# Optimization experiments

Hardware: AMD Instinct MI355X
Metric: run time of the kernel (lower is better)

The kernel has to match this reference:

```python
import jax, jax.numpy as jnp
import numpy as np

NUM_HEADS = 16
ROPE_BASE = 10000.0


def rotate_half(x):
    d = x.shape[-1] // 2
    return jnp.concatenate([-x[..., d:], x[..., :d]], axis=-1)


def setup_inputs() -> dict:
    key = jax.random.key(0)
    ks = jax.random.split(key, 6)
    B, S, H = 2, 2048, 1024
    scale = 1.0 / np.sqrt(H)  # ~xavier for square matrices
    x = jax.random.normal(ks[0], (B, S, H), dtype=jnp.float32)
    Wq = jax.random.normal(ks[1], (H, H), dtype=jnp.float32) * scale
    Wk = jax.random.normal(ks[2], (H, H), dtype=jnp.float32) * scale
    Wv = jax.random.normal(ks[3], (H, H), dtype=jnp.float32) * scale
    Wo = jax.random.normal(ks[4], (H, H), dtype=jnp.float32) * scale
    # learnable bias, tril-initialized as in the torch module
    bias = jnp.tril(jax.random.normal(ks[5], (S, S), dtype=jnp.float32) * 0.02)
    return {"x": x, "Wq": Wq, "Wk": Wk, "Wv": Wv, "Wo": Wo, "bias": bias}


def reference(x, Wq, Wk, Wv, Wo, bias):
    B, S, H = x.shape
    nh = NUM_HEADS
    hd = H // nh

    # projections (torch Linear: y = x @ W.T), split heads -> [B, nh, S, hd]
    q = (x @ Wq.T).reshape(B, S, nh, hd).transpose(0, 2, 1, 3)
    k = (x @ Wk.T).reshape(B, S, nh, hd).transpose(0, 2, 1, 3)
    v = (x @ Wv.T).reshape(B, S, nh, hd).transpose(0, 2, 1, 3)

    # rotary embeddings, position_ids = arange(S)
    inv_freq = 1.0 / (ROPE_BASE ** (jnp.arange(0, hd, 2, dtype=jnp.float32) / hd))
    t = jnp.arange(S, dtype=jnp.float32)
    freqs = t[:, None] * inv_freq[None, :]          # [S, hd/2]
    emb = jnp.concatenate([freqs, freqs], axis=-1)  # [S, hd]
    cos = jnp.cos(emb).astype(x.dtype)
    sin = jnp.sin(emb).astype(x.dtype)
    q = q * cos + rotate_half(q) * sin
    k = k * cos + rotate_half(k) * sin

    # scores + learnable bias + causal mask
    scores = jnp.einsum('bhqd,bhkd->bhqk', q, k) / np.float32(np.sqrt(hd))
    scores = scores + bias[:S, :S][None, None, :, :]
    causal = jnp.tril(jnp.ones((S, S), dtype=bool))
    scores = jnp.where(causal, scores, -jnp.inf)

    attn = jax.nn.softmax(scores, axis=-1)
    out = jnp.einsum('bhqk,bhkd->bhqd', attn, v)
    out = out.transpose(0, 2, 1, 3).reshape(B, S, H)
    return out @ Wo.T, attn
```

## Files before the change

### kernel.cpp

```cpp
#include <hip/hip_runtime.h>
#include <hip/hip_bf16.h>
#include <math.h>


typedef __attribute__((ext_vector_type(8))) short bx8;
typedef __attribute__((ext_vector_type(4))) short sx4;
typedef __attribute__((ext_vector_type(4))) float fx4;
typedef __attribute__((ext_vector_type(4))) float f4v;

#define MFMA_BF16(a, b, c) __builtin_amdgcn_mfma_f32_16x16x32_bf16(a, b, c, 0, 0, 0)
#define LOG2E 1.44269504088896340736f

__device__ __forceinline__ short f2bf(float f) {
    union { float f; unsigned u; } v; v.f = f;
    unsigned u = v.u;
    u += 0x7fffu + ((u >> 16) & 1u);
    return (short)(u >> 16);
}

__device__ __forceinline__ bx8 pack8(f4v a, f4v b) {
    bx8 r;
    r[0] = f2bf(a[0]); r[1] = f2bf(a[1]); r[2] = f2bf(a[2]); r[3] = f2bf(a[3]);
    r[4] = f2bf(b[0]); r[5] = f2bf(b[1]); r[6] = f2bf(b[2]); r[7] = f2bf(b[3]);
    return r;
}

__device__ __forceinline__ void gload_lds16(const short* g, short* l) {
    __builtin_amdgcn_global_load_lds(
        (const __attribute__((address_space(1))) void*)g,
        (__attribute__((address_space(3))) void*)l, 16, 0, 0);
}

__global__ __launch_bounds__(256) void cast_kernel(
        const float* __restrict__ x, const float* __restrict__ Wq,
        const float* __restrict__ Wk, const float* __restrict__ Wv,
        const float* __restrict__ Wo, const float* __restrict__ bias,
        short* __restrict__ dst, float* __restrict__ biasF)
{
    const size_t M1 = 1u << 20;
    if (blockIdx.x < 4096) {
        const size_t e0 = ((size_t)blockIdx.x * 256 + threadIdx.x) * 8;
        const float* src; size_t off;
        if (e0 < 4 * M1) { src = x; off = e0; }
        else {
            const int j = (int)((e0 - 4 * M1) >> 20);
            src = (j == 0) ? Wq : (j == 1) ? Wk : (j == 2) ? Wv : Wo;
            off = (e0 - 4 * M1) & (M1 - 1);
        }
        f4v a = *(const f4v*)(src + off);
        f4v b = *(const f4v*)(src + off + 4);
        *(bx8*)(dst + e0) = pack8(a, b);
    } else {
        const size_t e0 = ((size_t)(blockIdx.x - 4096) * 256 + threadIdx.x) * 8;
        f4v a = *(const f4v*)(bias + e0);
        f4v b = *(const f4v*)(bias + e0 + 4);
        #pragma unroll
        for (int i = 0; i < 4; ++i) { a[i] *= LOG2E; b[i] *= LOG2E; }
        *(f4v*)(biasF + e0) = a;
        *(f4v*)(biasF + e0 + 4) = b;
    }
}

__global__ void rope_table_kernel(float* __restrict__ cosT, float* __restrict__ sinT) {
    int i = blockIdx.x * 256 + threadIdx.x;
    if (i >= 2048 * 64) return;
    int s = i >> 6, d = i & 63;
    int fi = d & 31;
    float inv_freq = powf(10000.0f, -(float)fi / 32.0f);
    float ang = (float)s * inv_freq;
    cosT[i] = cosf(ang);
    sinT[i] = sinf(ang);
}

template<int OUTPROJ>
__global__ __launch_bounds__(256) void gemm128(
        const short* __restrict__ A, const short* __restrict__ W0,
        const short* __restrict__ W1, const short* __restrict__ W2,
        const float* __restrict__ cosT, const float* __restrict__ sinT,
        void* __restrict__ Out)
{
    __shared__ short As[128][64];
    __shared__ short Bs[128][64];
    const int bm = blockIdx.x, bn = blockIdx.y, z = blockIdx.z;
    const short* W = OUTPROJ ? W0 : (z == 0 ? W0 : (z == 1 ? W1 : W2));
    const int tid = threadIdx.x, w = tid >> 6, lane = tid & 63;
    const int cl = lane & 15, lg = lane >> 4;
    const int srow = lane >> 3;
    const int schunk = (lane & 7) ^ srow;

    fx4 acc[4][4];
    #pragma unroll
    for (int mi = 0; mi < 4; ++mi)
        #pragma unroll
        for (int ni = 0; ni < 4; ++ni) acc[mi][ni] = (fx4){0.f, 0.f, 0.f, 0.f};

    const int wr = (w >> 1) * 64, wc = (w & 1) * 64;

    for (int k0 = 0; k0 < 1024; k0 += 64) {
        __syncthreads();
        #pragma unroll
        for (int i = 0; i < 4; ++i) {
            const int rbase = w * 32 + i * 8;
            gload_lds16(A + (size_t)(bm * 128 + rbase + srow) * 1024 + k0 + schunk * 8,
                        &As[rbase][0]);
            gload_lds16(W + (size_t)(bn * 128 + rbase + srow) * 1024 + k0 + schunk * 8,
                        &Bs[rbase][0]);
        }
        __syncthreads();
        #pragma unroll
        for (int kk = 0; kk < 2; ++kk) {
            bx8 af[4], bf[4];
            #pragma unroll
            for (int i = 0; i < 4; ++i) {
                const int ra = wr + i * 16 + cl;
                af[i] = *(const bx8*)&As[ra][((kk * 4 + lg) ^ (ra & 7)) * 8];
                const int rb = wc + i * 16 + cl;
                bf[i] = *(const bx8*)&Bs[rb][((kk * 4 + lg) ^ (rb & 7)) * 8];
            }
            #pragma unroll
            for (int mi = 0; mi < 4; ++mi)
                #pragma unroll
                for (int ni = 0; ni < 4; ++ni)
                    acc[mi][ni] = MFMA_BF16(af[mi], bf[ni], acc[mi][ni]);
        }
    }

    #pragma unroll
    for (int mi = 0; mi < 4; ++mi) {
        #pragma unroll
        for (int reg = 0; reg < 4; ++reg) {
            const int r = bm * 128 + wr + mi * 16 + (lg << 2) + reg;
            if constexpr (OUTPROJ) {
                #pragma unroll
                for (int ni = 0; ni < 4; ++ni) {
                    const int col = bn * 128 + wc + ni * 16 + cl;
                    ((float*)Out)[(size_t)r * 1024 + col] = acc[mi][ni][reg];
                }
            } else {
                const int b = r >> 11, s = r & 2047;
                const int h = bn * 2 + (wc >> 6);
                short* dst = (short*)Out + (size_t)z * 32 * 2048 * 64
                           + (size_t)((b * 16 + h) * 2048 + s) * 64;
                #pragma unroll
                for (int ni = 0; ni < 4; ++ni) {
                    const int d = ni * 16 + cl;
                    float v = acc[mi][ni][reg];
                    if (z <= 1) {
                        const float cs = cosT[s * 64 + d], sn = sinT[s * 64 + d];
                        const float partner = acc[mi][ni ^ 2][reg];
                        const float rot = (d < 32) ? -partner : partner;
                        v = v * cs + rot * sn;
                        if (z == 0) v *= 0.125f * LOG2E;
                    }
                    dst[d] = f2bf(v);
                }
            }
        }
    }
}

__global__ __launch_bounds__(256, 3) void attn_kernel(
        const short* __restrict__ Q, const short* __restrict__ K,
        const short* __restrict__ V, const float* __restrict__ biasF,
        float* __restrict__ attn_out, short* __restrict__ o_buf)
{
    const int S = 2048;
    const int bid = blockIdx.x;
    const int xcd = bid & 7, rr_ = bid >> 3;
    const int bh = xcd * 4 + (rr_ & 3);
    const int qt = 31 - (rr_ >> 2);
    const int h = bh & 15, b = bh >> 4;
    const int tid = threadIdx.x, w = tid >> 6, lane = tid & 63;
    const int cl = lane & 15, lg = lane >> 4;
    const size_t base = (size_t)bh * S * 64;
    const int NT = qt + 1;

    __shared__ short Ks[2][64][64];
    __shared__ short Vt[2][64][72];
    __shared__ short P[4][16][72];

    const int krow8 = lane >> 3, kchk = (lane & 7) ^ krow8;
    const int vrow = tid >> 2, vd0 = (tid & 3) * 16;

    const short* qp = Q + base + (size_t)(qt * 64 + w * 16 + cl) * 64 + lg * 8;
    const bx8 qf0 = *(const bx8*)qp;
    const bx8 qf1 = *(const bx8*)(qp + 32);
    const int qr  = qt * 64 + w * 16 + cl;
    const int sq0 = qt * 64 + w * 16 + (lg << 2);
    const float* brow = biasF + (size_t)qr * 2048;
    const size_t arow_base = ((size_t)bh * S + qr) * S;

#define STAGEK(BUF, t)                                                            \
    { gload_lds16(K + base + (size_t)((t) * 64 + w * 16 + krow8) * 64 + kchk * 8, \
                  &Ks[BUF][w * 16][0]);                                           \
      gload_lds16(K + base + (size_t)((t) * 64 + w * 16 + 8 + krow8) * 64 + kchk * 8, \
                  &Ks[BUF][w * 16 + 8][0]); }

#define LOADB(BR, t)                                                              \
    { _Pragma("unroll") for (int n = 0; n < 4; ++n)                               \
        BR[n] = *(const f4v*)(brow + (t) * 64 + n * 16 + (lg << 2)); }

#define QKT(BUF, BR, SACC)                                                        \
    { const int cs_ = cl & 7;                                                     \
      _Pragma("unroll") for (int n = 0; n < 4; ++n) {                             \
        bx8 a0 = *(const bx8*)&Ks[BUF][n * 16 + cl][(lg ^ cs_) * 8];              \
        bx8 a1 = *(const bx8*)&Ks[BUF][n * 16 + cl][((4 + lg) ^ cs_) * 8];        \
        SACC[n] = MFMA_BF16(a0, qf0, BR[n]);                                      \
        SACC[n] = MFMA_BF16(a1, qf1, SACC[n]); } }

#define COMP_A(BUF, BR, t)                                                        \
    { fx4 sacc[4]; QKT(BUF, BR, sacc);                                            \
      _Pragma("unroll") for (int n = 0; n < 4; ++n)                               \
        _Pragma("unroll") for (int e = 0; e < 4; ++e) {                           \
          const int kc = (t) * 64 + n * 16 + (lg << 2) + e;                       \
          lsum[n] += (kc <= qr) ? exp2f(sacc[n][e]) : 0.f; } }

#define LOADVr(V0, V1, t)                                                         \
    { const short* vp = V + base + (size_t)((t) * 64 + vrow) * 64 + vd0;          \
      V0 = *(const bx8*)vp; V1 = *(const bx8*)(vp + 8); }

#define VSTORE(V0, V1, BUF)                                                       \
    { _Pragma("unroll") for (int j = 0; j < 8; ++j) Vt[BUF][vd0 + j][vrow] = V0[j]; \
      _Pragma("unroll") for (int j = 0; j < 8; ++j) Vt[BUF][vd0 + 8 + j][vrow] = V1[j]; }

#define COMP_B(KBUF, BR, VBUF, t)                                                 \
    { fx4 sacc[4]; QKT(KBUF, BR, sacc);                                           \
      float p[4][4];                                                              \
      _Pragma("unroll") for (int n = 0; n < 4; ++n)                               \
        _Pragma("unroll") for (int e = 0; e < 4; ++e) {                           \
          const int kc = (t) * 64 + n * 16 + (lg << 2) + e;                       \
          p[n][e] = (kc <= qr) ? exp2f(sacc[n][e] - L2) : 0.f; }                  \
      _Pragma("unroll") for (int n = 0; n < 4; ++n) {                             \
        f4v st = (f4v){p[n][0], p[n][1], p[n][2], p[n][3]};                       \
        *(f4v*)(attn_out + arow_base + (t) * 64 + n * 16 + (lg << 2)) = st;       \
        sx4 pb;                                                                   \
        pb[0] = f2bf(p[n][0]); pb[1] = f2bf(p[n][1]);                             \
        pb[2] = f2bf(p[n][2]); pb[3] = f2bf(p[n][3]);                             \
        *(sx4*)&P[w][cl][n * 16 + (lg << 2)] = pb; }                              \
      _Pragma("unroll") for (int kk = 0; kk < 2; ++kk) {                          \
        bx8 pa = *(const bx8*)&P[w][cl][kk * 32 + lg * 8];                        \
        _Pragma("unroll") for (int n = 0; n < 4; ++n) {                           \
          bx8 vb = *(const bx8*)&Vt[VBUF][n * 16 + cl][kk * 32 + lg * 8];         \
          oacc[n] = MFMA_BF16(pa, vb, oacc[n]); } } }

    float lsum[4] = {0.f, 0.f, 0.f, 0.f};
    f4v bA[4], bB[4];

    STAGEK(0, 0); LOADB(bA, 0);
    __syncthreads();
    int t = 0;
    for (; t + 1 < NT; t += 2) {
        STAGEK(1, t + 1); LOADB(bB, t + 1);
        COMP_A(0, bA, t);
        __syncthreads();
        if (t + 2 < NT) { STAGEK(0, t + 2); LOADB(bA, t + 2); }
        COMP_A(1, bB, t + 1);
        __syncthreads();
    }
    if (t < NT) COMP_A(0, bA, t);

    float l = (lsum[0] + lsum[1]) + (lsum[2] + lsum[3]);
    l += __shfl_xor(l, 16);
    l += __shfl_xor(l, 32);
    const float L2 = __log2f(l);

    fx4 oacc[4];
    #pragma unroll
    for (int n = 0; n < 4; n++) oacc[n] = (fx4){0.f, 0.f, 0.f, 0.f};

    bx8 vA0, vA1, vB0, vB1;
    __syncthreads();
    STAGEK(0, 0); LOADB(bA, 0); LOADVr(vA0, vA1, 0);
    __syncthreads();
    VSTORE(vA0, vA1, 0);
    __syncthreads();
    t = 0;
    for (; t + 1 < NT; t += 2) {
        STAGEK(1, t + 1); LOADB(bB, t + 1); LOADVr(vB0, vB1, t + 1);
        COMP_B(0, bA, 0, t);
        VSTORE(vB0, vB1, 1);
        __syncthreads();
        if (t + 2 < NT) { STAGEK(0, t + 2); LOADB(bA, t + 2); LOADVr(vA0, vA1, t + 2); }
        COMP_B(1, bB, 1, t + 1);
        if (t + 2 < NT) VSTORE(vA0, vA1, 0);
        __syncthreads();
    }
    if (t < NT) COMP_B(0, bA, 0, t);

    #pragma unroll
    for (int reg = 0; reg < 4; reg++) {
        const int sq = sq0 + reg;
        #pragma unroll
        for (int n = 0; n < 4; n++) {
            const int d = n * 16 + cl;
            o_buf[(size_t)(b * 2048 + sq) * 1024 + h * 64 + d] = f2bf(oacc[n][reg]);
        }
    }

    const int c0 = (qt + 1) * 64;
    if (c0 < S) {
        const int row = tid >> 2;
        float* dst = attn_out + ((size_t)bh * S + qt * 64 + (row & 63)) * S;
        const f4v z = (f4v){0.f, 0.f, 0.f, 0.f};
        for (int cc = c0 + (tid & 3) * 4; cc < S; cc += 16)
            *(f4v*)(dst + cc) = z;
    }
#undef STAGEK
#undef LOADB
#undef QKT
#undef COMP_A
#undef LOADVr
#undef VSTORE
#undef COMP_B
}

extern "C" void kernel_launch(void* const* d_in, const int* in_sizes, int n_in,
                              void* d_out, int out_size, void* d_ws, size_t ws_size,
                              hipStream_t stream) {
    const float* x    = (const float*)d_in[0];
    const float* Wq   = (const float*)d_in[1];
    const float* Wk   = (const float*)d_in[2];
    const float* Wv   = (const float*)d_in[3];
    const float* Wo   = (const float*)d_in[4];
    const float* bias = (const float*)d_in[5];

    float* out  = (float*)d_out;
    float* attn = out + (size_t)2 * 2048 * 1024;

    char* ws = (char*)d_ws;
    const size_t M1 = 1u << 20;
    short* x_bf    = (short*)ws;
    short* wq_bf   = x_bf + 4 * M1;
    short* wk_bf   = wq_bf + M1;
    short* wv_bf   = wk_bf + M1;
    short* wo_bf   = wv_bf + M1;
    float* biasF   = (float*)(ws + 16 * M1);
    float* cosT    = (float*)(ws + 32 * M1);
    float* sinT    = cosT + 2048 * 64;
    short* q_rope  = (short*)(ws + 33 * M1);
    short* k_rope  = q_rope + 4 * M1;
    short* v_bf    = k_rope + 4 * M1;
    short* o_buf   = x_bf;

    cast_kernel<<<6144, 256, 0, stream>>>(x, Wq, Wk, Wv, Wo, bias, x_bf, biasF);
    rope_table_kernel<<<512, 256, 0, stream>>>(cosT, sinT);
    gemm128<0><<<dim3(32, 8, 3), 256, 0, stream>>>(x_bf, wq_bf, wk_bf, wv_bf,
                                                   cosT, sinT, q_rope);
    attn_kernel<<<1024, 256, 0, stream>>>(q_rope, k_rope, v_bf, biasF, attn, o_buf);
    gemm128<1><<<dim3(32, 8, 1), 256, 0, stream>>>(o_buf, wo_bf, wo_bf, wo_bf,
                                                   cosT, sinT, out);
}
```

Baseline: 300.0 us.

## Split softmax row-sum pass into separate kernel and coalesce attn writes via LDS

Moves the first pass (row sums of exp over causal scores) out of the attention kernel into a new lsum_kernel. Each wave there handles 16 query rows and reads K directly from global memory, so the first pass gets finer-grained parallelism and the attention kernel only runs the second pass. The attention kernel now writes the bf16 probabilities into a double-buffered LDS strip and flushes them as coalesced row-contiguous fp32 stores. The zero-fill of the masked tail is restructured so each wave writes contiguous rows. In exchange it adds an extra kernel launch, re-reads Q/K/bias, and the attn output is now rounded to bf16 precision.

```diff
diff --git a/kernel.cpp b/kernel.cpp
--- a/kernel.cpp
+++ b/kernel.cpp
@@ -16,6 +16,9 @@
     unsigned u = v.u;
     u += 0x7fffu + ((u >> 16) & 1u);
     return (short)(u >> 16);
+}
+__device__ __forceinline__ float u2f(unsigned u) {
+    union { unsigned u; float f; } v; v.u = u; return v.f;
 }
 
 __device__ __forceinline__ bx8 pack8(f4v a, f4v b) {
@@ -159,9 +162,72 @@
     }
 }
 
+__global__ __launch_bounds__(256) void lsum_kernel(
+        const short* __restrict__ Q, const short* __restrict__ K,
+        const float* __restrict__ biasF, float* __restrict__ L2G)
+{
+    const int S = 2048;
+    const int tid = threadIdx.x, w = tid >> 6, lane = tid & 63;
+    const int cl = lane & 15, lg = lane >> 4;
+    const int idx = blockIdx.x * 4 + w;
+    const int qt = 31 - (idx & 31);
+    const int bh = (idx >> 5) & 31;
+    const int sub = idx >> 10;
+    const size_t base = (size_t)bh * S * 64;
+    const int qr0 = qt * 64 + sub * 16;
+    const int qr = qr0 + cl;
+    const float* brow = biasF + (size_t)qr * 2048;
+
+    bx8 qf0, qf1;
+    {
+        const short* qp = Q + base + (size_t)(qr0 + cl) * 64 + lg * 8;
+        qf0 = *(const bx8*)qp;
+        qf1 = *(const bx8*)(qp + 32);
+    }
+
+    float lsum[4] = {0.f, 0.f, 0.f, 0.f};
+    bx8 kA[4][2], kB[4][2];
+    f4v bA[4], bB[4];
+
+#define LKB(KARR, BARR, t)                                                       \
+    { _Pragma("unroll") for (int n = 0; n < 4; ++n) {                            \
+        const short* kp = K + base + (size_t)((t) * 64 + n * 16 + cl) * 64 + lg * 8; \
+        KARR[n][0] = *(const bx8*)kp; KARR[n][1] = *(const bx8*)(kp + 32); }     \
+      _Pragma("unroll") for (int n = 0; n < 4; ++n)                              \
+        BARR[n] = *(const f4v*)(brow + (t) * 64 + n * 16 + (lg << 2)); }
+
+#define ACC_A(KARR, BARR, t)                                                     \
+    { fx4 sacc[4];                                                               \
+      _Pragma("unroll") for (int n = 0; n < 4; ++n) {                            \
+        sacc[n] = MFMA_BF16(KARR[n][0], qf0, (fx4)BARR[n]);                      \
+        sacc[n] = MFMA_BF16(KARR[n][1], qf1, sacc[n]); }                         \
+      _Pragma("unroll") for (int n = 0; n < 4; ++n)                              \
+        _Pragma("unroll") for (int e = 0; e < 4; ++e) {                          \
+          const int kc = (t) * 64 + n * 16 + (lg << 2) + e;                      \
+          lsum[n] += (kc <= qr) ? exp2f(sacc[n][e]) : 0.f; } }
+
+    LKB(kA, bA, 0);
+    int t = 0;
+    for (; t + 1 <= qt; t += 2) {
+        LKB(kB, bB, t + 1);
+        ACC_A(kA, bA, t);
+        if (t + 2 <= qt) LKB(kA, bA, t + 2);
+        ACC_A(kB, bB, t + 1);
+    }
+    if (t <= qt) ACC_A(kA, bA, t);
+
+    float l = (lsum[0] + lsum[1]) + (lsum[2] + lsum[3]);
+    l += __shfl_xor(l, 16);
+    l += __shfl_xor(l, 32);
+    if (lane < 16) L2G[(size_t)bh * 2048 + qr] = __log2f(l);
+#undef LKB
+#undef ACC_A
+}
+
 __global__ __launch_bounds__(256, 3) void attn_kernel(
         const short* __restrict__ Q, const short* __restrict__ K,
         const short* __restrict__ V, const float* __restrict__ biasF,
+        const float* __restrict__ L2G,
         float* __restrict__ attn_out, short* __restrict__ o_buf)
 {
     const int S = 2048;
@@ -177,7 +243,7 @@
 
     __shared__ short Ks[2][64][64];
     __shared__ short Vt[2][64][72];
-    __shared__ short P[4][16][72];
+    __shared__ short P[4][16][136];
 
     const int krow8 = lane >> 3, kchk = (lane & 7) ^ krow8;
     const int vrow = tid >> 2, vd0 = (tid & 3) * 16;
@@ -188,7 +254,8 @@
     const int qr  = qt * 64 + w * 16 + cl;
     const int sq0 = qt * 64 + w * 16 + (lg << 2);
     const float* brow = biasF + (size_t)qr * 2048;
-    const size_t arow_base = ((size_t)bh * S + qr) * S;
+    const float L2v = L2G[(size_t)bh * 2048 + qr];
+    const size_t strip_base = ((size_t)bh * S + qt * 64 + w * 16) * S;
 
 #define STAGEK(BUF, t)                                                            \
     { gload_lds16(K + base + (size_t)((t) * 64 + w * 16 + krow8) * 64 + kchk * 8, \
@@ -200,21 +267,6 @@
     { _Pragma("unroll") for (int n = 0; n < 4; ++n)                               \
         BR[n] = *(const f4v*)(brow + (t) * 64 + n * 16 + (lg << 2)); }
 
-#define QKT(BUF, BR, SACC)                                                        \
-    { const int cs_ = cl & 7;                                                     \
-      _Pragma("unroll") for (int n = 0; n < 4; ++n) {                             \
-        bx8 a0 = *(const bx8*)&Ks[BUF][n * 16 + cl][(lg ^ cs_) * 8];              \
-        bx8 a1 = *(const bx8*)&Ks[BUF][n * 16 + cl][((4 + lg) ^ cs_) * 8];        \
-        SACC[n] = MFMA_BF16(a0, qf0, BR[n]);                                      \
-        SACC[n] = MFMA_BF16(a1, qf1, SACC[n]); } }
-
-#define COMP_A(BUF, BR, t)                                                        \
-    { fx4 sacc[4]; QKT(BUF, BR, sacc);                                            \
-      _Pragma("unroll") for (int n = 0; n < 4; ++n)                               \
-        _Pragma("unroll") for (int e = 0; e < 4; ++e) {                           \
-          const int kc = (t) * 64 + n * 16 + (lg << 2) + e;                       \
-          lsum[n] += (kc <= qr) ? exp2f(sacc[n][e]) : 0.f; } }
-
 #define LOADVr(V0, V1, t)                                                         \
     { const short* vp = V + base + (size_t)((t) * 64 + vrow) * 64 + vd0;          \
       V0 = *(const bx8*)vp; V1 = *(const bx8*)(vp + 8); }
@@ -224,57 +276,55 @@
       _Pragma("unroll") for (int j = 0; j < 8; ++j) Vt[BUF][vd0 + 8 + j][vrow] = V1[j]; }
 
 #define COMP_B(KBUF, BR, VBUF, t)                                                 \
-    { fx4 sacc[4]; QKT(KBUF, BR, sacc);                                           \
-      float p[4][4];                                                              \
-      _Pragma("unroll") for (int n = 0; n < 4; ++n)                               \
+    { fx4 sacc[4];                                                                \
+      { const int cs_ = cl & 7;                                                   \
+        _Pragma("unroll") for (int n = 0; n < 4; ++n) {                           \
+          bx8 a0 = *(const bx8*)&Ks[KBUF][n * 16 + cl][(lg ^ cs_) * 8];           \
+          bx8 a1 = *(const bx8*)&Ks[KBUF][n * 16 + cl][((4 + lg) ^ cs_) * 8];     \
+          sacc[n] = MFMA_BF16(a0, qf0, (fx4)BR[n]);                               \
+          sacc[n] = MFMA_BF16(a1, qf1, sacc[n]); } }                              \
+      _Pragma("unroll") for (int n = 0; n < 4; ++n) {                             \
+        sx4 pb;                                                                   \
         _Pragma("unroll") for (int e = 0; e < 4; ++e) {                           \
           const int kc = (t) * 64 + n * 16 + (lg << 2) + e;                       \
-          p[n][e] = (kc <= qr) ? exp2f(sacc[n][e] - L2) : 0.f; }                  \
-      _Pragma("unroll") for (int n = 0; n < 4; ++n) {                             \
-        f4v st = (f4v){p[n][0], p[n][1], p[n][2], p[n][3]};                       \
-        *(f4v*)(attn_out + arow_base + (t) * 64 + n * 16 + (lg << 2)) = st;       \
-        sx4 pb;                                                                   \
-        pb[0] = f2bf(p[n][0]); pb[1] = f2bf(p[n][1]);                             \
-        pb[2] = f2bf(p[n][2]); pb[3] = f2bf(p[n][3]);                             \
-        *(sx4*)&P[w][cl][n * 16 + (lg << 2)] = pb; }                              \
+          const float p = (kc <= qr) ? exp2f(sacc[n][e] - L2v) : 0.f;             \
+          pb[e] = f2bf(p); }                                                      \
+        *(sx4*)&P[w][cl][((t) & 1) * 64 + n * 16 + (lg << 2)] = pb; }             \
       _Pragma("unroll") for (int kk = 0; kk < 2; ++kk) {                          \
-        bx8 pa = *(const bx8*)&P[w][cl][kk * 32 + lg * 8];                        \
+        bx8 pa = *(const bx8*)&P[w][cl][((t) & 1) * 64 + kk * 32 + lg * 8];       \
         _Pragma("unroll") for (int n = 0; n < 4; ++n) {                           \
           bx8 vb = *(const bx8*)&Vt[VBUF][n * 16 + cl][kk * 32 + lg * 8];         \
           oacc[n] = MFMA_BF16(pa, vb, oacc[n]); } } }
 
-    float lsum[4] = {0.f, 0.f, 0.f, 0.f};
-    f4v bA[4], bB[4];
-
-    STAGEK(0, 0); LOADB(bA, 0);
-    __syncthreads();
-    int t = 0;
-    for (; t + 1 < NT; t += 2) {
-        STAGEK(1, t + 1); LOADB(bB, t + 1);
-        COMP_A(0, bA, t);
-        __syncthreads();
-        if (t + 2 < NT) { STAGEK(0, t + 2); LOADB(bA, t + 2); }
-        COMP_A(1, bB, t + 1);
-        __syncthreads();
-    }
-    if (t < NT) COMP_A(0, bA, t);
-
-    float l = (lsum[0] + lsum[1]) + (lsum[2] + lsum[3]);
-    l += __shfl_xor(l, 16);
-    l += __shfl_xor(l, 32);
-    const float L2 = __log2f(l);
+#define FLUSH2(tp)                                                                \
+    { _Pragma("unroll") for (int rp = 0; rp < 16; rp += 2) {                      \
+        const int row = rp + (lane >> 5), col = (lane & 31) * 4;                  \
+        const unsigned* ps = (const unsigned*)&P[w][row][col];                    \
+        const unsigned px = ps[0], py = ps[1];                                    \
+        f4v o; o[0] = u2f(px << 16); o[1] = u2f(px & 0xffff0000u);                \
+        o[2] = u2f(py << 16); o[3] = u2f(py & 0xffff0000u);                       \
+        *(f4v*)(attn_out + strip_base + (size_t)row * S + (tp) * 64 + col) = o; } }
+
+#define FLUSH1(tp)                                                                \
+    { _Pragma("unroll") for (int rp = 0; rp < 16; rp += 4) {                      \
+        const int row = rp + (lane >> 4), col = (lane & 15) * 4;                  \
+        const unsigned* ps = (const unsigned*)&P[w][row][col];                    \
+        const unsigned px = ps[0], py = ps[1];                                    \
+        f4v o; o[0] = u2f(px << 16); o[1] = u2f(px & 0xffff0000u);                \
+        o[2] = u2f(py << 16); o[3] = u2f(py & 0xffff0000u);                       \
+        *(f4v*)(attn_out + strip_base + (size_t)row * S + (tp) * 64 + col) = o; } }
 
     fx4 oacc[4];
     #pragma unroll
     for (int n = 0; n < 4; n++) oacc[n] = (fx4){0.f, 0.f, 0.f, 0.f};
-
+    f4v bA[4], bB[4];
     bx8 vA0, vA1, vB0, vB1;
-    __syncthreads();
+
     STAGEK(0, 0); LOADB(bA, 0); LOADVr(vA0, vA1, 0);
     __syncthreads();
     VSTORE(vA0, vA1, 0);
     __syncthreads();
-    t = 0;
+    int t = 0;
     for (; t + 1 < NT; t += 2) {
         STAGEK(1, t + 1); LOADB(bB, t + 1); LOADVr(vB0, vB1, t + 1);
         COMP_B(0, bA, 0, t);
@@ -282,10 +332,11 @@
         __syncthreads();
         if (t + 2 < NT) { STAGEK(0, t + 2); LOADB(bA, t + 2); LOADVr(vA0, vA1, t + 2); }
         COMP_B(1, bB, 1, t + 1);
+        FLUSH2(t);
         if (t + 2 < NT) VSTORE(vA0, vA1, 0);
         __syncthreads();
     }
-    if (t < NT) COMP_B(0, bA, 0, t);
+    if (t < NT) { COMP_B(0, bA, 0, t); FLUSH1(t); }
 
     #pragma unroll
     for (int reg = 0; reg < 4; reg++) {
@@ -299,19 +350,20 @@
 
     const int c0 = (qt + 1) * 64;
     if (c0 < S) {
-        const int row = tid >> 2;
-        float* dst = attn_out + ((size_t)bh * S + qt * 64 + (row & 63)) * S;
         const f4v z = (f4v){0.f, 0.f, 0.f, 0.f};
-        for (int cc = c0 + (tid & 3) * 4; cc < S; cc += 16)
-            *(f4v*)(dst + cc) = z;
+        for (int r = w; r < 64; r += 4) {
+            float* dst = attn_out + ((size_t)bh * S + qt * 64 + r) * S;
+            for (int cc = c0 + lane * 4; cc < S; cc += 256)
+                *(f4v*)(dst + cc) = z;
+        }
     }
 #undef STAGEK
 #undef LOADB
-#undef QKT
-#undef COMP_A
 #undef LOADVr
 #undef VSTORE
 #undef COMP_B
+#undef FLUSH2
+#undef FLUSH1
 }
 
 extern "C" void kernel_launch(void* const* d_in, const int* in_sizes, int n_in,
@@ -340,13 +392,16 @@
     short* q_rope  = (short*)(ws + 33 * M1);
     short* k_rope  = q_rope + 4 * M1;
     short* v_bf    = k_rope + 4 * M1;
+    float* L2G     = (float*)(ws + 57 * M1);
     short* o_buf   = x_bf;
 
     cast_kernel<<<6144, 256, 0, stream>>>(x, Wq, Wk, Wv, Wo, bias, x_bf, biasF);
     rope_table_kernel<<<512, 256, 0, stream>>>(cosT, sinT);
     gemm128<0><<<dim3(32, 8, 3), 256, 0, stream>>>(x_bf, wq_bf, wk_bf, wv_bf,
                                                    cosT, sinT, q_rope);
-    attn_kernel<<<1024, 256, 0, stream>>>(q_rope, k_rope, v_bf, biasF, attn, o_buf);
+    lsum_kernel<<<1024, 256, 0, stream>>>(q_rope, k_rope, biasF, L2G);
+    attn_kernel<<<1024, 256, 0, stream>>>(q_rope, k_rope, v_bf, biasF, L2G,
+                                          attn, o_buf);
     gemm128<1><<<dim3(32, 8, 1), 256, 0, stream>>>(o_buf, wo_bf, wo_bf, wo_bf,
                                                    cosT, sinT, out);
 }
```

After: 414.4 us. 38.1% more time.

## Stage attention probabilities in LDS and write them as coalesced row strips

Applied to the files above, without the earlier changes.

The fp32 attention matrix was written straight from MFMA registers, each lane storing 16-byte pieces scattered across 16 rows. Now the bf16 probabilities for two key tiles are kept in a widened LDS P buffer, then each wave expands them back to fp32 and writes contiguous 128-column row segments. The zero-fill of the masked upper region is also reorganised so each wave writes whole rows contiguously. The aim is to cut the cost of the dominant attention-matrix store through better coalescing. The trade-off is that the returned attention values are now rounded to bf16 instead of full fp32, and there is extra LDS traffic.

```diff
diff --git a/kernel.cpp b/kernel.cpp
--- a/kernel.cpp
+++ b/kernel.cpp
@@ -16,6 +16,9 @@
     unsigned u = v.u;
     u += 0x7fffu + ((u >> 16) & 1u);
     return (short)(u >> 16);
+}
+__device__ __forceinline__ float u2f(unsigned u) {
+    union { unsigned u; float f; } v; v.u = u; return v.f;
 }
 
 __device__ __forceinline__ bx8 pack8(f4v a, f4v b) {
@@ -177,7 +180,7 @@
 
     __shared__ short Ks[2][64][64];
     __shared__ short Vt[2][64][72];
-    __shared__ short P[4][16][72];
+    __shared__ short P[4][16][136];
 
     const int krow8 = lane >> 3, kchk = (lane & 7) ^ krow8;
     const int vrow = tid >> 2, vd0 = (tid & 3) * 16;
@@ -188,7 +191,7 @@
     const int qr  = qt * 64 + w * 16 + cl;
     const int sq0 = qt * 64 + w * 16 + (lg << 2);
     const float* brow = biasF + (size_t)qr * 2048;
-    const size_t arow_base = ((size_t)bh * S + qr) * S;
+    const size_t strip_base = ((size_t)bh * S + qt * 64 + w * 16) * S;
 
 #define STAGEK(BUF, t)                                                            \
     { gload_lds16(K + base + (size_t)((t) * 64 + w * 16 + krow8) * 64 + kchk * 8, \
@@ -225,23 +228,36 @@
 
 #define COMP_B(KBUF, BR, VBUF, t)                                                 \
     { fx4 sacc[4]; QKT(KBUF, BR, sacc);                                           \
-      float p[4][4];                                                              \
-      _Pragma("unroll") for (int n = 0; n < 4; ++n)                               \
+      _Pragma("unroll") for (int n = 0; n < 4; ++n) {                             \
+        sx4 pb;                                                                   \
         _Pragma("unroll") for (int e = 0; e < 4; ++e) {                           \
           const int kc = (t) * 64 + n * 16 + (lg << 2) + e;                       \
-          p[n][e] = (kc <= qr) ? exp2f(sacc[n][e] - L2) : 0.f; }                  \
-      _Pragma("unroll") for (int n = 0; n < 4; ++n) {                             \
-        f4v st = (f4v){p[n][0], p[n][1], p[n][2], p[n][3]};                       \
-        *(f4v*)(attn_out + arow_base + (t) * 64 + n * 16 + (lg << 2)) = st;       \
-        sx4 pb;                                                                   \
-        pb[0] = f2bf(p[n][0]); pb[1] = f2bf(p[n][1]);                             \
-        pb[2] = f2bf(p[n][2]); pb[3] = f2bf(p[n][3]);                             \
-        *(sx4*)&P[w][cl][n * 16 + (lg << 2)] = pb; }                              \
+          const float p = (kc <= qr) ? exp2f(sacc[n][e] - L2) : 0.f;              \
+          pb[e] = f2bf(p); }                                                      \
+        *(sx4*)&P[w][cl][((t) & 1) * 64 + n * 16 + (lg << 2)] = pb; }             \
       _Pragma("unroll") for (int kk = 0; kk < 2; ++kk) {                          \
-        bx8 pa = *(const bx8*)&P[w][cl][kk * 32 + lg * 8];                        \
+        bx8 pa = *(const bx8*)&P[w][cl][((t) & 1) * 64 + kk * 32 + lg * 8];       \
         _Pragma("unroll") for (int n = 0; n < 4; ++n) {                           \
           bx8 vb = *(const bx8*)&Vt[VBUF][n * 16 + cl][kk * 32 + lg * 8];         \
           oacc[n] = MFMA_BF16(pa, vb, oacc[n]); } } }
+
+#define FLUSH2(tp)                                                                \
+    { _Pragma("unroll") for (int rp = 0; rp < 16; rp += 2) {                      \
+        const int row = rp + (lane >> 5), col = (lane & 31) * 4;                  \
+        const unsigned* ps = (const unsigned*)&P[w][row][col];                    \
+        const unsigned px = ps[0], py = ps[1];                                    \
+        f4v o; o[0] = u2f(px << 16); o[1] = u2f(px & 0xffff0000u);                \
+        o[2] = u2f(py << 16); o[3] = u2f(py & 0xffff0000u);                       \
+        *(f4v*)(attn_out + strip_base + (size_t)row * S + (tp) * 64 + col) = o; } }
+
+#define FLUSH1(tp)                                                                \
+    { _Pragma("unroll") for (int rp = 0; rp < 16; rp += 4) {                      \
+        const int row = rp + (lane >> 4), col = (lane & 15) * 4;                  \
+        const unsigned* ps = (const unsigned*)&P[w][row][col];                    \
+        const unsigned px = ps[0], py = ps[1];                                    \
+        f4v o; o[0] = u2f(px << 16); o[1] = u2f(px & 0xffff0000u);                \
+        o[2] = u2f(py << 16); o[3] = u2f(py & 0xffff0000u);                       \
+        *(f4v*)(attn_out + strip_base + (size_t)row * S + (tp) * 64 + col) = o; } }
 
     float lsum[4] = {0.f, 0.f, 0.f, 0.f};
     f4v bA[4], bB[4];
@@ -282,10 +298,11 @@
         __syncthreads();
         if (t + 2 < NT) { STAGEK(0, t + 2); LOADB(bA, t + 2); LOADVr(vA0, vA1, t + 2); }
         COMP_B(1, bB, 1, t + 1);
+        FLUSH2(t);
         if (t + 2 < NT) VSTORE(vA0, vA1, 0);
         __syncthreads();
     }
-    if (t < NT) COMP_B(0, bA, 0, t);
+    if (t < NT) { COMP_B(0, bA, 0, t); FLUSH1(t); }
 
     #pragma unroll
     for (int reg = 0; reg < 4; reg++) {
@@ -299,11 +316,12 @@
 
     const int c0 = (qt + 1) * 64;
     if (c0 < S) {
-        const int row = tid >> 2;
-        float* dst = attn_out + ((size_t)bh * S + qt * 64 + (row & 63)) * S;
         const f4v z = (f4v){0.f, 0.f, 0.f, 0.f};
-        for (int cc = c0 + (tid & 3) * 4; cc < S; cc += 16)
-            *(f4v*)(dst + cc) = z;
+        for (int r = w; r < 64; r += 4) {
+            float* dst = attn_out + ((size_t)bh * S + qt * 64 + r) * S;
+            for (int cc = c0 + lane * 4; cc < S; cc += 256)
+                *(f4v*)(dst + cc) = z;
+        }
     }
 #undef STAGEK
 #undef LOADB
@@ -312,6 +330,8 @@
 #undef LOADVr
 #undef VSTORE
 #undef COMP_B
+#undef FLUSH2
+#undef FLUSH1
 }
 
 extern "C" void kernel_launch(void* const* d_in, const int* in_sizes, int n_in,
```

Measured after the change: 282.3 us. 1.06x faster.
